# Optimization experiments

Measured on AMD Instinct MI355X. Metric: run time of the kernel, lower is better.

The kernel has to match this reference:

```python
import jax, jax.numpy as jnp
import numpy as np

B, S, D = 2, 2048, 4096
H, KV, HD = 32, 8, 128
THETA = 10000.0


def rotate_half(x):
    x1, x2 = x[..., : HD // 2], x[..., HD // 2 :]
    return jnp.concatenate((-x2, x1), axis=-1)


def setup_inputs() -> dict:
    key = jax.random.key(0)
    ks = jax.random.split(key, 8)
    s = 1.0 / np.sqrt(D)
    return {
        "hidden_states": jax.random.normal(ks[0], (B, S, D), jnp.float32),
        "modality_indicators": jax.random.randint(ks[1], (B, S), 0, 2, jnp.int64 if jax.config.jax_enable_x64 else jnp.int32),
        "position_ids": jnp.arange(S, dtype=jnp.int32),
        "Wq": jax.random.normal(ks[2], (D, H * HD), jnp.float32) * s,
        "Wk0": jax.random.normal(ks[3], (D, KV * HD), jnp.float32) * s,
        "Wk1": jax.random.normal(ks[4], (D, KV * HD), jnp.float32) * s,
        "Wv0": jax.random.normal(ks[5], (D, KV * HD), jnp.float32) * s,
        "Wv1": jax.random.normal(ks[6], (D, KV * HD), jnp.float32) * s,
        "Wo": jax.random.normal(ks[7], (H * HD, D), jnp.float32) * s,
    }


def reference(hidden_states, modality_indicators, position_ids, Wq, Wk0, Wk1, Wv0, Wv1, Wo):
    x = hidden_states
    # Multiway (modality-routed) k/v projections: per-token select between two linears.
    sel = (modality_indicators == 1)[..., None]  # [B,S,1]
    q = x @ Wq                                   # [B,S,H*HD]
    k = jnp.where(sel, x @ Wk1, x @ Wk0)         # [B,S,KV*HD]
    v = jnp.where(sel, x @ Wv1, x @ Wv0)

    q = q.reshape(B, S, H, HD).transpose(0, 2, 1, 3)    # [B,H,S,HD]
    k = k.reshape(B, S, KV, HD).transpose(0, 2, 1, 3)   # [B,KV,S,HD]
    v = v.reshape(B, S, KV, HD).transpose(0, 2, 1, 3)

    # RoPE cache and application (emb = cat(freqs, freqs))
    inv_freq = 1.0 / (THETA ** (jnp.arange(0, HD, 2, dtype=jnp.float32) / HD))
    freqs = position_ids.astype(jnp.float32)[:, None] * inv_freq[None, :]   # [S,HD/2]
    emb = jnp.concatenate((freqs, freqs), axis=-1)                          # [S,HD]
    cos = jnp.cos(emb)[None, None, :, :]                                    # [1,1,S,HD]
    sin = jnp.sin(emb)[None, None, :, :]
    q = q * cos + rotate_half(q) * sin
    k = k * cos + rotate_half(k) * sin

    # GQA: repeat kv heads
    n_rep = H // KV
    k = jnp.repeat(k, n_rep, axis=1)  # [B,H,S,HD]
    v = jnp.repeat(v, n_rep, axis=1)

    scores = jnp.einsum("bhqd,bhkd->bhqk", q, k) / np.sqrt(HD)
    causal = jnp.tril(jnp.ones((S, S), dtype=bool))
    scores = jnp.where(causal[None, None], scores, jnp.finfo(scores.dtype).min)
    attn = jax.nn.softmax(scores, axis=-1)
    ctx = jnp.einsum("bhqk,bhkd->bhqd", attn, v)            # [B,H,S,HD]
    ctx = ctx.transpose(0, 2, 1, 3).reshape(B, S, H * HD)
    return ctx @ Wo
```

## Files before the change

### kernel.cpp

```cpp
#include <hip/hip_runtime.h>

typedef unsigned short u16;
typedef unsigned int   u32;
using bf16x8 = __attribute__((ext_vector_type(8))) __bf16;
using f32x4  = __attribute__((ext_vector_type(4))) float;
using f32x16 = __attribute__((ext_vector_type(16))) float;
using u32x4  = __attribute__((ext_vector_type(4))) unsigned int;
using ushort8 = __attribute__((ext_vector_type(8))) unsigned short;


__device__ __forceinline__ u16 f2bf(float f) {
  u32 u = __builtin_bit_cast(u32, f);
  return (u16)((u + 0x7fffu + ((u >> 16) & 1u)) >> 16);
}
__device__ __forceinline__ float bf2f(u16 h) {
  return __builtin_bit_cast(float, (u32)h << 16);
}
__device__ __forceinline__ f32x4 mfma16(bf16x8 a, bf16x8 b, f32x4 c) {
  return __builtin_amdgcn_mfma_f32_16x16x32_bf16(a, b, c, 0, 0, 0);
}
__device__ __forceinline__ f32x16 mfma32(bf16x8 a, bf16x8 b, f32x16 c) {
  return __builtin_amdgcn_mfma_f32_32x32x16_bf16(a, b, c, 0, 0, 0);
}
__device__ __forceinline__ f32x16 zero16() {
  f32x16 z;
#pragma unroll
  for (int i = 0; i < 16; ++i) z[i] = 0.f;
  return z;
}
__device__ __forceinline__ void g2l16(const void* gp, void* lp) {
  __builtin_amdgcn_global_load_lds(
      (__attribute__((address_space(1))) void*)(void*)gp,
      (__attribute__((address_space(3))) void*)lp, 16, 0, 0);
}

__global__ void k_cvt(const float* __restrict__ in, u16* __restrict__ out, int n4) {
  int i = blockIdx.x * 256 + threadIdx.x;
  if (i >= n4) return;
  float4 v = ((const float4*)in)[i];
  ushort4 o;
  o.x = f2bf(v.x); o.y = f2bf(v.y); o.z = f2bf(v.z); o.w = f2bf(v.w);
  ((ushort4*)out)[i] = o;
}

__device__ __forceinline__ void tcvt_tile(const float* __restrict__ in, u16* __restrict__ out,
                                          int K, int N, int nt, int kt, u16 (*t)[72]) {
  const int n0 = nt * 64, k0 = kt * 64;
  const int tid = threadIdx.x;
  const int r = tid >> 2, c4 = (tid & 3) * 16;
  const float* src = in + (size_t)(k0 + r) * N + n0 + c4;
#pragma unroll
  for (int q = 0; q < 4; ++q) {
    float4 v = *(const float4*)(src + 4 * q);
    t[c4 + 4 * q + 0][r] = f2bf(v.x);
    t[c4 + 4 * q + 1][r] = f2bf(v.y);
    t[c4 + 4 * q + 2][r] = f2bf(v.z);
    t[c4 + 4 * q + 3][r] = f2bf(v.w);
  }
  __syncthreads();
  u16* dst = out + (size_t)(n0 + r) * K + k0 + c4;
#pragma unroll
  for (int hh = 0; hh < 2; ++hh)
    *(ushort8*)(dst + 8 * hh) = *(const ushort8*)(&t[r][c4 + 8 * hh]);
}

__global__ __launch_bounds__(256) void k_tcvt(const float* __restrict__ in, u16* __restrict__ out,
                                              int K, int N) {
  __shared__ u16 t[64][72];
  tcvt_tile(in, out, K, N, blockIdx.x, blockIdx.y, t);
}

__global__ __launch_bounds__(256) void k_tcvt5(const float* __restrict__ Wq, const float* __restrict__ Wk0,
                                               const float* __restrict__ Wv0, const float* __restrict__ Wk1,
                                               const float* __restrict__ Wv1, u16* __restrict__ WqT,
                                               u16* __restrict__ Wkv0T, u16* __restrict__ Wkv1T) {
  __shared__ u16 t[64][72];
  int bid = blockIdx.x;
  if (bid < 4096) {
    tcvt_tile(Wq, WqT, 4096, 4096, bid & 63, bid >> 6, t);
  } else {
    int r = bid - 4096;
    int mat = r >> 10, rr = r & 1023;
    const float* src = (mat == 0) ? Wk0 : (mat == 1) ? Wv0 : (mat == 2) ? Wk1 : Wv1;
    u16* dst = (mat == 0) ? Wkv0T : (mat == 1) ? (Wkv0T + (size_t)1024 * 4096)
                                  : (mat == 2) ? Wkv1T : (Wkv1T + (size_t)1024 * 4096);
    tcvt_tile(src, dst, 4096, 1024, rr & 15, rr >> 4, t);
  }
}

__global__ void k_scan(const int* __restrict__ mod, int* __restrict__ perm, int* __restrict__ meta) {
  __shared__ int ps[1024];
  const int b = blockIdx.x, t = threadIdx.x;
  perm[b * 2304 + t] = -1;
  perm[b * 2304 + 1024 + t] = -1;
  if (t < 256) perm[b * 2304 + 2048 + t] = -1;
  const int i0 = 2 * t, i1 = 2 * t + 1;
  const int f0 = (mod[b * 2048 + i0] != 1) ? 1 : 0;
  const int f1 = (mod[b * 2048 + i1] != 1) ? 1 : 0;
  const int sum = f0 + f1;
  ps[t] = sum;
  __syncthreads();
  for (int off = 1; off < 1024; off <<= 1) {
    int v = (t >= off) ? ps[t - off] : 0;
    __syncthreads();
    ps[t] += v;
    __syncthreads();
  }
  const int total0 = ps[1023];
  const int excl = ps[t] - sum;
  const int nt0 = (total0 + 255) >> 8;
  const int off1 = nt0 * 256;
  const int s0 = f0 ? excl : off1 + (i0 - excl);
  const int s1 = f1 ? (excl + f0) : off1 + (i1 - (excl + f0));
  perm[b * 2304 + s0] = i0;
  perm[b * 2304 + s1] = i1;
  if (t == 0) { meta[b * 2] = total0; meta[b * 2 + 1] = nt0; }
}

#define TILE_BODY(T, VMLIT, DOSTAGE)                                         \
  {                                                                          \
    asm volatile("s_waitcnt vmcnt(" VMLIT ")" ::: "memory");                 \
    __builtin_amdgcn_s_barrier();                                            \
    __builtin_amdgcn_sched_barrier(0);                                       \
    const u16* base_ = lds + ((T) & 3) * 16384;                              \
    bf16x8 bfr[4], afr[4];                                                   \
    _Pragma("unroll")                                                        \
    for (int nf = 0; nf < 4; ++nf)                                           \
      bfr[nf] = *(const bf16x8*)(base_ + boff + nf * 512);                   \
    _Pragma("unroll")                                                        \
    for (int mf = 0; mf < 4; ++mf)                                           \
      afr[mf] = *(const bf16x8*)(base_ + aoff + mf * 512);                   \
    if (DOSTAGE) stage((T) + 3);                                             \
    __builtin_amdgcn_s_setprio(1);                                           \
    _Pragma("unroll")                                                        \
    for (int mf = 0; mf < 4; ++mf)                                           \
      _Pragma("unroll")                                                      \
      for (int nf = 0; nf < 4; ++nf)                                         \
        acc[mf][nf] = mfma16(afr[mf], bfr[nf], acc[mf][nf]);                 \
    __builtin_amdgcn_s_setprio(0);                                           \
  }

#define GEMM_MAIN_LOOP()                                                     \
  stage(0); stage(1); stage(2);                                              \
  for (int t = 0; t < 125; ++t) TILE_BODY(t, "4", true);                     \
  TILE_BODY(125, "4", false);                                                \
  TILE_BODY(126, "2", false);                                                \
  TILE_BODY(127, "0", false);

__global__ __launch_bounds__(1024, 4) void k_gemm8(const u16* __restrict__ A, const u16* __restrict__ Bt,
                                                   float* __restrict__ Cp) {
  __shared__ u16 lds[4 * 16384];
  const int tid = threadIdx.x, wid = tid >> 6, l = tid & 63, g = l >> 4, li = l & 15;
  const int wr = wid >> 2, wc = wid & 3;
  const int bid = blockIdx.x;
  const int swz = (bid & 7) * 32 + (bid >> 3);
  const int m0 = (swz >> 4) * 256, n0 = (swz & 15) * 256;

  const int srow = wid * 16 + (l >> 2);
  const int sgg = (l & 3) ^ ((l >> 3) & 3);
  const u16* pA = A + (size_t)(m0 + srow) * 4096 + sgg * 8;
  const u16* pB = Bt + (size_t)(n0 + srow) * 4096 + sgg * 8;

  auto stage = [&](int t) {
    u16* da = (u16*)lds + (t & 3) * 16384 + wid * 512;
    g2l16(pA + t * 32, da);
    g2l16(pB + t * 32, da + 8192);
  };

  const int lsl8 = (g ^ ((li >> 1) & 3)) * 8;
  const int aoff = (wr * 64 + li) * 32 + lsl8;
  const int boff = 8192 + (wc * 64 + li) * 32 + lsl8;

  const f32x4 vzero = {0.f, 0.f, 0.f, 0.f};
  f32x4 acc[4][4];
#pragma unroll
  for (int m = 0; m < 4; ++m)
#pragma unroll
    for (int n = 0; n < 4; ++n) acc[m][n] = vzero;

  GEMM_MAIN_LOOP();

#pragma unroll
  for (int mf = 0; mf < 4; ++mf)
#pragma unroll
    for (int nf = 0; nf < 4; ++nf)
#pragma unroll
      for (int j = 0; j < 4; ++j) {
        int row = m0 + wr * 64 + mf * 16 + g * 4 + j;
        int col = n0 + wc * 64 + nf * 16 + li;
        Cp[(size_t)row * 4096 + col] = acc[mf][nf][j];
      }
}

__global__ __launch_bounds__(1024, 4) void k_gemmQKV(const u16* __restrict__ Xb, const u16* __restrict__ WqT,
                                                     const u16* __restrict__ B0, const u16* __restrict__ B1,
                                                     const int* __restrict__ perm, const int* __restrict__ meta,
                                                     u16* __restrict__ Qr, u16* __restrict__ Ksel,
                                                     u16* __restrict__ Vsel) {
  __shared__ u16 lds[4 * 16384];
  const int tid = threadIdx.x, wid = tid >> 6, l = tid & 63, g = l >> 4, li = l & 15;
  const int wr = wid >> 2, wc = wid & 3;
  const int bid = blockIdx.x;
  const bool isQ = bid < 256;

  const int srow = wid * 16 + (l >> 2);
  const int sgg = (l & 3) ^ ((l >> 3) & 3);

  int m0 = 0, n0 = 0, bb = 0, tm = 0;
  const u16 *pA, *pB;
  if (isQ) {
    const int swz = (bid & 7) * 32 + (bid >> 3);
    m0 = (swz >> 4) * 256; n0 = (swz & 15) * 256;
    pA = Xb + (size_t)(m0 + srow) * 4096 + sgg * 8;
    pB = WqT + (size_t)(n0 + srow) * 4096 + sgg * 8;
  } else {
    const int kb = bid - 256;
    const int seg = kb >> 3;
    n0 = (kb & 7) * 256;
    bb = seg / 9; tm = seg % 9;
    const int nt0 = meta[bb * 2 + 1];
    const u16* Bt = (tm >= nt0) ? B1 : B0;
    int t0 = perm[bb * 2304 + tm * 256 + srow];
    if (t0 < 0) t0 = 0;
    pA = Xb + ((size_t)bb * 2048 + t0) * 4096 + sgg * 8;
    pB = Bt + (size_t)(n0 + srow) * 4096 + sgg * 8;
  }

  auto stage = [&](int t) {
    u16* da = (u16*)lds + (t & 3) * 16384 + wid * 512;
    g2l16(pA + t * 32, da);
    g2l16(pB + t * 32, da + 8192);
  };

  const int lsl8 = (g ^ ((li >> 1) & 3)) * 8;
  const int aoff = (wr * 64 + li) * 32 + lsl8;
  const int boff = 8192 + (wc * 64 + li) * 32 + lsl8;

  const f32x4 vzero = {0.f, 0.f, 0.f, 0.f};
  f32x4 acc[4][4];
#pragma unroll
  for (int m = 0; m < 4; ++m)
#pragma unroll
    for (int n = 0; n < 4; ++n) acc[m][n] = vzero;

  GEMM_MAIN_LOOP();

  if (isQ) {
#pragma unroll
    for (int mf = 0; mf < 4; ++mf)
#pragma unroll
      for (int nf = 0; nf < 4; ++nf)
#pragma unroll
        for (int j = 0; j < 4; ++j) {
          int row = m0 + wr * 64 + mf * 16 + g * 4 + j;
          int col = n0 + wc * 64 + nf * 16 + li;
          int b = row >> 11, s = row & 2047, h = col >> 7, d = col & 127;
          Qr[(((size_t)(b * 32 + h)) * 2048 + s) * 128 + d] = f2bf(acc[mf][nf][j]);
        }
  } else {
#pragma unroll
    for (int mf = 0; mf < 4; ++mf)
#pragma unroll
      for (int nf = 0; nf < 4; ++nf)
#pragma unroll
        for (int j = 0; j < 4; ++j) {
          int slot = tm * 256 + wr * 64 + mf * 16 + g * 4 + j;
          int tok = perm[bb * 2304 + slot];
          if (tok >= 0) {
            int col = n0 + wc * 64 + nf * 16 + li;
            int kv = col >> 10, hh = (col >> 7) & 7, d = col & 127;
            u16* dst = (kv ? Vsel : Ksel) + (((size_t)(bb * 8 + hh)) * 2048 + tok) * 128 + d;
            *dst = f2bf(acc[mf][nf][j]);
          }
        }
  }
}

__global__ __launch_bounds__(256) void k_ropekv(u16* __restrict__ Q, const u16* __restrict__ Ks,
                                                const u16* __restrict__ Vs, const int* __restrict__ pos,
                                                u16* __restrict__ Kr, u16* __restrict__ Vt) {
  __shared__ u16 Vl[64][136];
  const int bid = blockIdx.x;
  const int tid = threadIdx.x, l = tid & 63;
  const float invf = expf((float)l * -0.14391156831212787f);
  if (bid < 32768) {
    int row = bid * 4 + (tid >> 6);
    int s = row & 2047;
    u16* p = Q + (size_t)row * 128;
    float x1 = bf2f(p[l]), x2 = bf2f(p[l + 64]);
    float ang = (float)pos[s] * invf;
    float cs = cosf(ang), sn = sinf(ang);
    const float sc = 0.08838834764831845f;
    p[l] = f2bf((x1 * cs - x2 * sn) * sc);
    p[l + 64] = f2bf((x2 * cs + x1 * sn) * sc);
  } else {
    int blk = bid - 32768;
    int st = blk & 31, kvh = (blk >> 5) & 7, b = blk >> 8;
    int s0 = st * 64;
    int wid = tid >> 6;
    size_t slab = (size_t)(b * 8 + kvh) * 2048;
    for (int rr = 0; rr < 16; ++rr) {
      int r = wid * 16 + rr;
      int s = s0 + r;
      const u16* ks = Ks + (slab + s) * 128;
      const u16* vs = Vs + (slab + s) * 128;
      float ang = (float)pos[s] * invf;
      float cs = cosf(ang), sn = sinf(ang);
      float x1 = bf2f(ks[l]), x2 = bf2f(ks[l + 64]);
      u16* kd = Kr + (slab + s) * 128;
      kd[l] = f2bf(x1 * cs - x2 * sn);
      kd[l + 64] = f2bf(x2 * cs + x1 * sn);
      Vl[r][l] = vs[l];
      Vl[r][l + 64] = vs[l + 64];
    }
    __syncthreads();
    int d = tid >> 1, si0 = (tid & 1) * 32;
    u16* vd = Vt + ((size_t)(b * 8 + kvh) * 128 + d) * 2048 + s0 + si0;
#pragma unroll
    for (int k4 = 0; k4 < 8; ++k4) {
      ushort4 o;
      o.x = Vl[si0 + k4 * 4 + 0][d];
      o.y = Vl[si0 + k4 * 4 + 1][d];
      o.z = Vl[si0 + k4 * 4 + 2][d];
      o.w = Vl[si0 + k4 * 4 + 3][d];
      *(ushort4*)(vd + k4 * 4) = o;
    }
  }
}

__global__ __launch_bounds__(256, 2) void k_attn(const u16* __restrict__ Q, const u16* __restrict__ Kr,
                                                 const u16* __restrict__ Vt, u16* __restrict__ ctx) {
  __shared__ u16 Kl[2 * 64 * 128];
  __shared__ u16 Vl[2 * 128 * 64];
  const int bh = blockIdx.x;
  const int p = blockIdx.y;
  const int b = bh >> 5, h = bh & 31, kvh = h >> 2;
  const int tid = threadIdx.x, w = tid >> 6, l = tid & 63;
  const int lo5 = l & 31, hi = l >> 5;
  const bool hib = hi != 0;
  const size_t kvslab = (size_t)(b * 8 + kvh) * 2048;
  const u16* Kg = Kr + kvslab * 128;
  const u16* Vg = Vt + kvslab * 128;
  const float L2E = 1.4426950408889634f;

  auto stage = [&](int kt, int bi) {
#pragma unroll
    for (int i = 0; i < 4; ++i) {
      int c = w * 4 + i;
      int slot = c * 1024 + l * 16;
      {
        int row = slot >> 8;
        int inner = (slot & 255) ^ ((row & 15) << 4);
        g2l16((const char*)Kg + kt * 16384 + row * 256 + inner,
              (char*)Kl + bi * 16384 + c * 1024);
      }
      {
        int row = slot >> 7;
        int inner = (slot & 127) ^ ((row & 7) << 4);
        g2l16((const char*)Vg + (size_t)row * 4096 + kt * 128 + inner,
              (char*)Vl + bi * 16384 + c * 1024);
      }
    }
  };

  for (int hf = 0; hf < 2; ++hf) {
    const int qi = hf ? (15 - p) : p;
    const int q0 = qi * 128;
    const int qlane = q0 + w * 32 + lo5;
    const u16* qrow = Q + ((size_t)bh * 2048 + qlane) * 128;
    bf16x8 qf[8];
#pragma unroll
    for (int kk = 0; kk < 8; ++kk) qf[kk] = *(const bf16x8*)(qrow + kk * 16 + hi * 8);

    f32x16 ot[4];
#pragma unroll
    for (int i = 0; i < 4; ++i) ot[i] = zero16();
    float m = -1e30f, ls = 0.f;

    const int nkt = 2 * qi + 2;
    stage(0, 0);
    stage(1, 1);
    for (int kt = 0; kt < nkt; ++kt) {
      if (kt + 1 < nkt) {
        asm volatile("s_waitcnt vmcnt(8)" ::: "memory");
      } else {
        asm volatile("s_waitcnt vmcnt(0)" ::: "memory");
      }
      __builtin_amdgcn_s_barrier();
      __builtin_amdgcn_sched_barrier(0);
      const char* kbase = (const char*)Kl + (kt & 1) * 16384;
      const char* vbase = (const char*)Vl + (kt & 1) * 16384;
      const int ktb = kt * 64;
      if (ktb <= q0 + w * 32 + 31) {
        f32x16 st[2];
        st[0] = zero16(); st[1] = zero16();
#pragma unroll
        for (int kk = 0; kk < 8; ++kk) {
          bf16x8 kfr[2];
#pragma unroll
          for (int mf = 0; mf < 2; ++mf) {
            int row = mf * 32 + lo5;
            kfr[mf] = *(const bf16x8*)(kbase + row * 256 + ((kk * 32 + hi * 16) ^ ((row & 15) << 4)));
          }
          __builtin_amdgcn_s_setprio(1);
          st[0] = mfma32(kfr[0], qf[kk], st[0]);
          st[1] = mfma32(kfr[1], qf[kk], st[1]);
          __builtin_amdgcn_s_setprio(0);
        }
        if (ktb + 63 > q0 + w * 32) {
#pragma unroll
          for (int mf = 0; mf < 2; ++mf)
#pragma unroll
            for (int r = 0; r < 16; ++r) {
              int kg = ktb + mf * 32 + (r & 3) + 8 * (r >> 2) + 4 * hi;
              if (kg > qlane) st[mf][r] = -3.0e38f;
            }
        }
        float t[16];
#pragma unroll
        for (int r = 0; r < 16; ++r) t[r] = fmaxf(st[0][r], st[1][r]);
#pragma unroll
        for (int s = 8; s >= 1; s >>= 1)
#pragma unroll
          for (int r = 0; r < s; ++r) t[r] = fmaxf(t[r], t[r + s]);
        float pmax = fmaxf(t[0], __shfl_xor(t[0], 32));
        if (!__all(pmax <= m + 8.f)) {
          float nm = fmaxf(m, pmax);
          float resc = exp2f((m - nm) * L2E);
          m = nm;
          ls *= resc;
#pragma unroll
          for (int i = 0; i < 4; ++i)
#pragma unroll
            for (int r = 0; r < 16; ++r) ot[i][r] *= resc;
        }
#pragma unroll
        for (int mf = 0; mf < 2; ++mf)
#pragma unroll
          for (int r = 0; r < 16; ++r) st[mf][r] = exp2f((st[mf][r] - m) * L2E);
        float u[16];
#pragma unroll
        for (int r = 0; r < 16; ++r) u[r] = st[0][r] + st[1][r];
#pragma unroll
        for (int s = 8; s >= 1; s >>= 1)
#pragma unroll
          for (int r = 0; r < s; ++r) u[r] += u[r + s];
        ls += u[0] + __shfl_xor(u[0], 32);
        u32 pkv[16];
#pragma unroll
        for (int mf = 0; mf < 2; ++mf)
#pragma unroll
          for (int tt = 0; tt < 8; ++tt) {
            u32 r;
            asm("v_cvt_pk_bf16_f32 %0, %1, %2" : "=v"(r) : "v"(st[mf][2 * tt]), "v"(st[mf][2 * tt + 1]));
            pkv[mf * 8 + tt] = r;
          }
        bf16x8 pfrag[4];
#pragma unroll
        for (int kk = 0; kk < 4; ++kk) {
          int c = (kk >> 1) * 8 + (kk & 1) * 4;
          u32 m0 = hib ? pkv[c + 2] : pkv[c + 0];
          u32 m1 = hib ? pkv[c + 3] : pkv[c + 1];
          u32 s0 = hib ? pkv[c + 0] : pkv[c + 2];
          u32 s1 = hib ? pkv[c + 1] : pkv[c + 3];
          u32 r0 = (u32)__shfl_xor((int)s0, 32);
          u32 r1 = (u32)__shfl_xor((int)s1, 32);
          u32x4 wv = {hib ? r0 : m0, hib ? r1 : m1, hib ? m0 : r0, hib ? m1 : r1};
          pfrag[kk] = __builtin_bit_cast(bf16x8, wv);
        }
#pragma unroll
        for (int mfV = 0; mfV < 4; ++mfV) {
          int row = mfV * 32 + lo5;
          const char* vb = vbase + row * 128;
          int sw = (row & 7) << 4;
          bf16x8 vf[4];
#pragma unroll
          for (int kk = 0; kk < 4; ++kk)
            vf[kk] = *(const bf16x8*)(vb + ((kk * 32 + hi * 16) ^ sw));
          __builtin_amdgcn_s_setprio(1);
#pragma unroll
          for (int kk = 0; kk < 4; ++kk) ot[mfV] = mfma32(vf[kk], pfrag[kk], ot[mfV]);
          __builtin_amdgcn_s_setprio(0);
        }
      }
      __builtin_amdgcn_s_barrier();
      if (kt + 2 < nkt) stage(kt + 2, kt & 1);
    }
    float inv = 1.0f / ls;
    u16* crow = ctx + ((size_t)(b * 2048) + qlane) * 4096 + h * 128;
#pragma unroll
    for (int mfV = 0; mfV < 4; ++mfV)
#pragma unroll
      for (int rq = 0; rq < 4; ++rq) {
        ushort4 o4;
        o4.x = f2bf(ot[mfV][rq * 4 + 0] * inv);
        o4.y = f2bf(ot[mfV][rq * 4 + 1] * inv);
        o4.z = f2bf(ot[mfV][rq * 4 + 2] * inv);
        o4.w = f2bf(ot[mfV][rq * 4 + 3] * inv);
        *(ushort4*)(crow + mfV * 32 + rq * 8 + hi * 4) = o4;
      }
  }
}

extern "C" void kernel_launch(void* const* d_in, const int* in_sizes, int n_in,
                              void* d_out, int out_size, void* d_ws, size_t ws_size,
                              hipStream_t stream) {
  (void)in_sizes; (void)n_in; (void)out_size; (void)ws_size;
  const float* X   = (const float*)d_in[0];
  const int*   mod = (const int*)d_in[1];
  const int*   pos = (const int*)d_in[2];
  const float* Wq  = (const float*)d_in[3];
  const float* Wk0 = (const float*)d_in[4];
  const float* Wk1 = (const float*)d_in[5];
  const float* Wv0 = (const float*)d_in[6];
  const float* Wv1 = (const float*)d_in[7];
  const float* Wo  = (const float*)d_in[8];
  float* out = (float*)d_out;

  u16* p = (u16*)d_ws;
  auto take = [&](size_t n) { u16* r = p; p += n; return r; };
  u16* Xb    = take(16777216);
  u16* WqT   = take(16777216);
  u16* WoT   = take(16777216);
  u16* Wkv0T = take(8388608);
  u16* Wkv1T = take(8388608);
  u16* Qr    = take(16777216);
  u16* Ksel  = take(4194304);
  u16* Vsel  = take(4194304);
  int* perm  = (int*)take(9216);
  int* meta  = (int*)take(64);
  u16* Kr  = WqT;
  u16* Vtr = WqT + 4194304;
  u16* ctx = Xb;

  k_cvt<<<dim3(16384), 256, 0, stream>>>(X, Xb, 4194304);
  k_scan<<<dim3(2), 1024, 0, stream>>>(mod, perm, meta);
  k_tcvt5<<<dim3(8192), 256, 0, stream>>>(Wq, Wk0, Wv0, Wk1, Wv1, WqT, Wkv0T, Wkv1T);

  k_gemmQKV<<<dim3(400), 1024, 0, stream>>>(Xb, WqT, Wkv0T, Wkv1T, perm, meta, Qr, Ksel, Vsel);

  k_ropekv<<<dim3(33280), 256, 0, stream>>>(Qr, Ksel, Vsel, pos, Kr, Vtr);

  k_attn<<<dim3(64, 8), 256, 0, stream>>>(Qr, Kr, Vtr, ctx);

  k_tcvt<<<dim3(64, 64), 256, 0, stream>>>(Wo, WoT, 4096, 4096);

  k_gemm8<<<dim3(256), 1024, 0, stream>>>(ctx, WoT, out);
}
```

Before: 550.7 us.

## Double-buffer QKV GEMM LDS and regroup attention blocks by KV head

The QKV projection GEMM moves from a 4-deep LDS ring with 3 tiles in flight to a 2-buffer scheme that stages the next-next tile after a second barrier, halving its shared memory footprint, which could raise occupancy but adds a barrier per tile and shortens prefetch distance. The attention launch becomes 1D with a block index mapping that places the four query heads sharing a KV head (and both batches) adjacently, aiming to improve L2 reuse of K/V tiles. Work per block is unchanged.

```diff
diff --git a/kernel.cpp b/kernel.cpp
--- a/kernel.cpp
+++ b/kernel.cpp
@@ -147,6 +147,36 @@
   TILE_BODY(126, "2", false);                                                \
   TILE_BODY(127, "0", false);
 
+#define TILE_BODY2(T, VMLIT, DOSTAGE)                                        \
+  {                                                                          \
+    asm volatile("s_waitcnt vmcnt(" VMLIT ")" ::: "memory");                 \
+    __builtin_amdgcn_s_barrier();                                            \
+    __builtin_amdgcn_sched_barrier(0);                                       \
+    const u16* base_ = lds + ((T) & 1) * 16384;                              \
+    bf16x8 bfr[4], afr[4];                                                   \
+    _Pragma("unroll")                                                        \
+    for (int nf = 0; nf < 4; ++nf)                                           \
+      bfr[nf] = *(const bf16x8*)(base_ + boff + nf * 512);                   \
+    _Pragma("unroll")                                                        \
+    for (int mf = 0; mf < 4; ++mf)                                           \
+      afr[mf] = *(const bf16x8*)(base_ + aoff + mf * 512);                   \
+    __builtin_amdgcn_s_setprio(1);                                           \
+    _Pragma("unroll")                                                        \
+    for (int mf = 0; mf < 4; ++mf)                                           \
+      _Pragma("unroll")                                                      \
+      for (int nf = 0; nf < 4; ++nf)                                         \
+        acc[mf][nf] = mfma16(afr[mf], bfr[nf], acc[mf][nf]);                 \
+    __builtin_amdgcn_s_setprio(0);                                           \
+    __builtin_amdgcn_s_barrier();                                            \
+    if (DOSTAGE) stage((T) + 2);                                             \
+  }
+
+#define GEMM_MAIN_LOOP2()                                                    \
+  stage(0); stage(1);                                                        \
+  for (int t = 0; t < 126; ++t) TILE_BODY2(t, "2", true);                    \
+  TILE_BODY2(126, "2", false);                                               \
+  TILE_BODY2(127, "0", false);
+
 __global__ __launch_bounds__(1024, 4) void k_gemm8(const u16* __restrict__ A, const u16* __restrict__ Bt,
                                                    float* __restrict__ Cp) {
   __shared__ u16 lds[4 * 16384];
@@ -197,7 +227,7 @@
                                                      const int* __restrict__ perm, const int* __restrict__ meta,
                                                      u16* __restrict__ Qr, u16* __restrict__ Ksel,
                                                      u16* __restrict__ Vsel) {
-  __shared__ u16 lds[4 * 16384];
+  __shared__ u16 lds[2 * 16384];
   const int tid = threadIdx.x, wid = tid >> 6, l = tid & 63, g = l >> 4, li = l & 15;
   const int wr = wid >> 2, wc = wid & 3;
   const int bid = blockIdx.x;
@@ -227,7 +257,7 @@
   }
 
   auto stage = [&](int t) {
-    u16* da = (u16*)lds + (t & 3) * 16384 + wid * 512;
+    u16* da = (u16*)lds + (t & 1) * 16384 + wid * 512;
     g2l16(pA + t * 32, da);
     g2l16(pB + t * 32, da + 8192);
   };
@@ -243,7 +273,7 @@
 #pragma unroll
     for (int n = 0; n < 4; ++n) acc[m][n] = vzero;
 
-  GEMM_MAIN_LOOP();
+  GEMM_MAIN_LOOP2();
 
   if (isQ) {
 #pragma unroll
@@ -332,9 +362,12 @@
                                                  const u16* __restrict__ Vt, u16* __restrict__ ctx) {
   __shared__ u16 Kl[2 * 64 * 128];
   __shared__ u16 Vl[2 * 128 * 64];
-  const int bh = blockIdx.x;
-  const int p = blockIdx.y;
-  const int b = bh >> 5, h = bh & 31, kvh = h >> 2;
+  const int id = blockIdx.x;
+  const int gkv = id & 15, j = id >> 4;
+  const int b = gkv >> 3, kvh = gkv & 7;
+  const int h = kvh * 4 + (j & 3);
+  const int p = j >> 2;
+  const int bh = b * 32 + h;
   const int tid = threadIdx.x, w = tid >> 6, l = tid & 63;
   const int lo5 = l & 31, hi = l >> 5;
   const bool hib = hi != 0;
@@ -541,7 +574,7 @@
 
   k_ropekv<<<dim3(33280), 256, 0, stream>>>(Qr, Ksel, Vsel, pos, Kr, Vtr);
 
-  k_attn<<<dim3(64, 8), 256, 0, stream>>>(Qr, Kr, Vtr, ctx);
+  k_attn<<<dim3(512), 256, 0, stream>>>(Qr, Kr, Vtr, ctx);
 
   k_tcvt<<<dim3(64, 64), 256, 0, stream>>>(Wo, WoT, 4096, 4096);
 
```

Result: slower. 566.1 us (+2.8%).

## Restructure GEMMs to 8-wave 256x256 tiles with quadrant-interleaved ping-pong pipeline

Applied to the files above, without the earlier changes.

Both GEMM kernels move from 16 waves with a four-deep single-stage pipeline to 8 waves that each compute a 128x64 sub-tile. The K step grows to 64 and LDS is split into two ping-pong buffers, with loads and MFMAs interleaved in quadrant order under barriers. The aim is more MFMA work per LDS read and finer-grained overlap of global-to-LDS copies with compute, at the cost of more accumulator registers per wave. Separately, the attention grid is flattened so the four query heads sharing a KV head launch next to each other, which should improve L2 reuse of K/V.

```diff
diff --git a/kernel.cpp b/kernel.cpp
--- a/kernel.cpp
+++ b/kernel.cpp
@@ -117,102 +117,142 @@
   if (t == 0) { meta[b * 2] = total0; meta[b * 2 + 1] = nt0; }
 }
 
-#define TILE_BODY(T, VMLIT, DOSTAGE)                                         \
-  {                                                                          \
-    asm volatile("s_waitcnt vmcnt(" VMLIT ")" ::: "memory");                 \
-    __builtin_amdgcn_s_barrier();                                            \
-    __builtin_amdgcn_sched_barrier(0);                                       \
-    const u16* base_ = lds + ((T) & 3) * 16384;                              \
-    bf16x8 bfr[4], afr[4];                                                   \
-    _Pragma("unroll")                                                        \
-    for (int nf = 0; nf < 4; ++nf)                                           \
-      bfr[nf] = *(const bf16x8*)(base_ + boff + nf * 512);                   \
-    _Pragma("unroll")                                                        \
-    for (int mf = 0; mf < 4; ++mf)                                           \
-      afr[mf] = *(const bf16x8*)(base_ + aoff + mf * 512);                   \
-    if (DOSTAGE) stage((T) + 3);                                             \
-    __builtin_amdgcn_s_setprio(1);                                           \
-    _Pragma("unroll")                                                        \
-    for (int mf = 0; mf < 4; ++mf)                                           \
-      _Pragma("unroll")                                                      \
-      for (int nf = 0; nf < 4; ++nf)                                         \
-        acc[mf][nf] = mfma16(afr[mf], bfr[nf], acc[mf][nf]);                 \
-    __builtin_amdgcn_s_setprio(0);                                           \
-  }
-
-#define GEMM_MAIN_LOOP()                                                     \
-  stage(0); stage(1); stage(2);                                              \
-  for (int t = 0; t < 125; ++t) TILE_BODY(t, "4", true);                     \
-  TILE_BODY(125, "4", false);                                                \
-  TILE_BODY(126, "2", false);                                                \
-  TILE_BODY(127, "0", false);
-
-__global__ __launch_bounds__(1024, 4) void k_gemm8(const u16* __restrict__ A, const u16* __restrict__ Bt,
-                                                   float* __restrict__ Cp) {
-  __shared__ u16 lds[4 * 16384];
+#define BARSB() { __builtin_amdgcn_s_barrier(); __builtin_amdgcn_sched_barrier(0); }
+#define VMC(N)  asm volatile("s_waitcnt vmcnt(" #N ")" ::: "memory")
+
+#define READ_A(MH, SL) { _Pragma("unroll") for (int mf_ = 0; mf_ < 4; ++mf_) {       \
+    const char* a_ = (const char*)lds8 + (SL)*65536 + (MH)*16384 + (arow + mf_*16)*128; \
+    afr[mf_][0] = *(const bf16x8*)(a_ + swc0);                                        \
+    afr[mf_][1] = *(const bf16x8*)(a_ + swc1); } }
+
+#define READ_B(NH, SL) { _Pragma("unroll") for (int nf_ = 0; nf_ < 2; ++nf_) {       \
+    const char* b_ = (const char*)lds8 + (SL)*65536 + 32768 + (NH)*16384 + (brow + nf_*16)*128; \
+    bfr[nf_][0] = *(const bf16x8*)(b_ + swc0);                                        \
+    bfr[nf_][1] = *(const bf16x8*)(b_ + swc1); } }
+
+#define MM16(MH, NH) { __builtin_amdgcn_s_setprio(1);                                 \
+  _Pragma("unroll") for (int mf_ = 0; mf_ < 4; ++mf_)                                 \
+    _Pragma("unroll") for (int nf_ = 0; nf_ < 2; ++nf_) {                             \
+      acc[MH][mf_][NH][nf_] = mfma16(afr[mf_][0], bfr[nf_][0], acc[MH][mf_][NH][nf_]); \
+      acc[MH][mf_][NH][nf_] = mfma16(afr[mf_][1], bfr[nf_][1], acc[MH][mf_][NH][nf_]); } \
+  __builtin_amdgcn_s_setprio(0); }
+
+#define STAGE_A(T, MH) { int ts_ = (T) < 64 ? (T) : 63;                               \
+    char* d_ = (char*)lds8 + ((T)&1)*65536 + (MH)*16384 + wid*1024;                   \
+    g2l16(pA0[MH] + ts_*64, d_); g2l16(pA1[MH] + ts_*64, d_ + 8192); }
+
+#define STAGE_B(T, NH) { int ts_ = (T) < 64 ? (T) : 63;                               \
+    char* d_ = (char*)lds8 + ((T)&1)*65536 + 32768 + (NH)*16384 + wid*1024;           \
+    g2l16(pB0[NH] + ts_*64, d_); g2l16(pB1[NH] + ts_*64, d_ + 8192); }
+
+#define G8_MAINLOOP()                                                                 \
+  STAGE_A(0,0); STAGE_B(0,1); STAGE_A(0,1); STAGE_B(0,0);                             \
+  STAGE_A(1,0); STAGE_B(1,1); STAGE_A(1,1);                                           \
+  VMC(6); BARSB();                                                                    \
+  for (int i_ = 0; i_ < 32; ++i_) {                                                   \
+    const int ta_ = 2 * i_;                                                           \
+    READ_A(0,0); READ_B(0,0); STAGE_B(ta_+1, 0); BARSB(); MM16(0,0); BARSB();         \
+    READ_B(1,0);              STAGE_A(ta_+2, 0); BARSB(); MM16(0,1); BARSB();         \
+    READ_A(1,0);              STAGE_B(ta_+2, 1); BARSB(); MM16(1,1); BARSB();         \
+    READ_B(0,0);              STAGE_A(ta_+2, 1); BARSB(); MM16(1,0); VMC(4); BARSB(); \
+    READ_A(0,1); READ_B(0,1); STAGE_B(ta_+2, 0); BARSB(); MM16(0,0); BARSB();         \
+    READ_B(1,1);              STAGE_A(ta_+3, 0); BARSB(); MM16(0,1); BARSB();         \
+    READ_A(1,1);              STAGE_B(ta_+3, 1); BARSB(); MM16(1,1); BARSB();         \
+    READ_B(0,1);              STAGE_A(ta_+3, 1); BARSB(); MM16(1,0); VMC(4); BARSB(); \
+  }
+
+__global__ __launch_bounds__(512, 2) void k_gemm8(const u16* __restrict__ A, const u16* __restrict__ Bt,
+                                                  float* __restrict__ Cp) {
+  __shared__ u16 lds8[65536];
   const int tid = threadIdx.x, wid = tid >> 6, l = tid & 63, g = l >> 4, li = l & 15;
   const int wr = wid >> 2, wc = wid & 3;
   const int bid = blockIdx.x;
   const int swz = (bid & 7) * 32 + (bid >> 3);
   const int m0 = (swz >> 4) * 256, n0 = (swz & 15) * 256;
 
-  const int srow = wid * 16 + (l >> 2);
-  const int sgg = (l & 3) ^ ((l >> 3) & 3);
-  const u16* pA = A + (size_t)(m0 + srow) * 4096 + sgg * 8;
-  const u16* pB = Bt + (size_t)(n0 + srow) * 4096 + sgg * 8;
-
-  auto stage = [&](int t) {
-    u16* da = (u16*)lds + (t & 3) * 16384 + wid * 512;
-    g2l16(pA + t * 32, da);
-    g2l16(pB + t * 32, da + 8192);
-  };
-
-  const int lsl8 = (g ^ ((li >> 1) & 3)) * 8;
-  const int aoff = (wr * 64 + li) * 32 + lsl8;
-  const int boff = 8192 + (wc * 64 + li) * 32 + lsl8;
-
+  const int swc0 = (g * 16) ^ ((li & 7) << 4);
+  const int swc1 = (64 + g * 16) ^ ((li & 7) << 4);
+  const int arow = wr * 64 + li;
+  const int brow = wc * 32 + li;
+
+  const int l8a = tid * 16, l8b = 8192 + tid * 16;
+  const int oa = l8a ^ (((l8a >> 7) & 7) << 4), ob = l8b ^ (((l8b >> 7) & 7) << 4);
+  const int rl0 = oa >> 7, cb0 = oa & 127, rl1 = ob >> 7, cb1 = ob & 127;
+  const int RA0 = (rl0 >> 6) * 128 + (rl0 & 63), RA1 = (rl1 >> 6) * 128 + (rl1 & 63);
+  const int CB0 = (rl0 >> 5) * 64 + (rl0 & 31), CB1 = (rl1 >> 5) * 64 + (rl1 & 31);
+  const u16 *pA0[2], *pA1[2], *pB0[2], *pB1[2];
+#pragma unroll
+  for (int mh = 0; mh < 2; ++mh) {
+    pA0[mh] = A + (size_t)(m0 + RA0 + mh * 64) * 4096 + cb0 / 2;
+    pA1[mh] = A + (size_t)(m0 + RA1 + mh * 64) * 4096 + cb1 / 2;
+    pB0[mh] = Bt + (size_t)(n0 + CB0 + mh * 32) * 4096 + cb0 / 2;
+    pB1[mh] = Bt + (size_t)(n0 + CB1 + mh * 32) * 4096 + cb1 / 2;
+  }
+
+  bf16x8 afr[4][2], bfr[2][2];
   const f32x4 vzero = {0.f, 0.f, 0.f, 0.f};
-  f32x4 acc[4][4];
-#pragma unroll
-  for (int m = 0; m < 4; ++m)
-#pragma unroll
-    for (int n = 0; n < 4; ++n) acc[m][n] = vzero;
-
-  GEMM_MAIN_LOOP();
-
-#pragma unroll
-  for (int mf = 0; mf < 4; ++mf)
-#pragma unroll
-    for (int nf = 0; nf < 4; ++nf)
-#pragma unroll
-      for (int j = 0; j < 4; ++j) {
-        int row = m0 + wr * 64 + mf * 16 + g * 4 + j;
-        int col = n0 + wc * 64 + nf * 16 + li;
-        Cp[(size_t)row * 4096 + col] = acc[mf][nf][j];
-      }
-}
-
-__global__ __launch_bounds__(1024, 4) void k_gemmQKV(const u16* __restrict__ Xb, const u16* __restrict__ WqT,
-                                                     const u16* __restrict__ B0, const u16* __restrict__ B1,
-                                                     const int* __restrict__ perm, const int* __restrict__ meta,
-                                                     u16* __restrict__ Qr, u16* __restrict__ Ksel,
-                                                     u16* __restrict__ Vsel) {
-  __shared__ u16 lds[4 * 16384];
+  f32x4 acc[2][4][2][2];
+#pragma unroll
+  for (int a = 0; a < 2; ++a)
+#pragma unroll
+    for (int b = 0; b < 4; ++b)
+#pragma unroll
+      for (int c = 0; c < 2; ++c)
+#pragma unroll
+        for (int d = 0; d < 2; ++d) acc[a][b][c][d] = vzero;
+
+  G8_MAINLOOP();
+
+#pragma unroll
+  for (int mh = 0; mh < 2; ++mh)
+#pragma unroll
+    for (int mf = 0; mf < 4; ++mf)
+#pragma unroll
+      for (int nh = 0; nh < 2; ++nh)
+#pragma unroll
+        for (int nf = 0; nf < 2; ++nf)
+#pragma unroll
+          for (int j = 0; j < 4; ++j) {
+            int row = m0 + wr * 128 + mh * 64 + mf * 16 + g * 4 + j;
+            int col = n0 + wc * 64 + nh * 32 + nf * 16 + li;
+            Cp[(size_t)row * 4096 + col] = acc[mh][mf][nh][nf][j];
+          }
+}
+
+__global__ __launch_bounds__(512, 2) void k_gemmQKV(const u16* __restrict__ Xb, const u16* __restrict__ WqT,
+                                                    const u16* __restrict__ B0, const u16* __restrict__ B1,
+                                                    const int* __restrict__ perm, const int* __restrict__ meta,
+                                                    u16* __restrict__ Qr, u16* __restrict__ Ksel,
+                                                    u16* __restrict__ Vsel) {
+  __shared__ u16 lds8[65536];
   const int tid = threadIdx.x, wid = tid >> 6, l = tid & 63, g = l >> 4, li = l & 15;
   const int wr = wid >> 2, wc = wid & 3;
   const int bid = blockIdx.x;
   const bool isQ = bid < 256;
 
-  const int srow = wid * 16 + (l >> 2);
-  const int sgg = (l & 3) ^ ((l >> 3) & 3);
+  const int swc0 = (g * 16) ^ ((li & 7) << 4);
+  const int swc1 = (64 + g * 16) ^ ((li & 7) << 4);
+  const int arow = wr * 64 + li;
+  const int brow = wc * 32 + li;
+
+  const int l8a = tid * 16, l8b = 8192 + tid * 16;
+  const int oa = l8a ^ (((l8a >> 7) & 7) << 4), ob = l8b ^ (((l8b >> 7) & 7) << 4);
+  const int rl0 = oa >> 7, cb0 = oa & 127, rl1 = ob >> 7, cb1 = ob & 127;
+  const int RA0 = (rl0 >> 6) * 128 + (rl0 & 63), RA1 = (rl1 >> 6) * 128 + (rl1 & 63);
+  const int CB0 = (rl0 >> 5) * 64 + (rl0 & 31), CB1 = (rl1 >> 5) * 64 + (rl1 & 31);
 
   int m0 = 0, n0 = 0, bb = 0, tm = 0;
-  const u16 *pA, *pB;
+  const u16 *pA0[2], *pA1[2], *pB0[2], *pB1[2];
   if (isQ) {
     const int swz = (bid & 7) * 32 + (bid >> 3);
     m0 = (swz >> 4) * 256; n0 = (swz & 15) * 256;
-    pA = Xb + (size_t)(m0 + srow) * 4096 + sgg * 8;
-    pB = WqT + (size_t)(n0 + srow) * 4096 + sgg * 8;
+#pragma unroll
+    for (int mh = 0; mh < 2; ++mh) {
+      pA0[mh] = Xb + (size_t)(m0 + RA0 + mh * 64) * 4096 + cb0 / 2;
+      pA1[mh] = Xb + (size_t)(m0 + RA1 + mh * 64) * 4096 + cb1 / 2;
+      pB0[mh] = WqT + (size_t)(n0 + CB0 + mh * 32) * 4096 + cb0 / 2;
+      pB1[mh] = WqT + (size_t)(n0 + CB1 + mh * 32) * 4096 + cb1 / 2;
+    }
   } else {
     const int kb = bid - 256;
     const int seg = kb >> 3;
@@ -220,59 +260,68 @@
     bb = seg / 9; tm = seg % 9;
     const int nt0 = meta[bb * 2 + 1];
     const u16* Bt = (tm >= nt0) ? B1 : B0;
-    int t0 = perm[bb * 2304 + tm * 256 + srow];
-    if (t0 < 0) t0 = 0;
-    pA = Xb + ((size_t)bb * 2048 + t0) * 4096 + sgg * 8;
-    pB = Bt + (size_t)(n0 + srow) * 4096 + sgg * 8;
-  }
-
-  auto stage = [&](int t) {
-    u16* da = (u16*)lds + (t & 3) * 16384 + wid * 512;
-    g2l16(pA + t * 32, da);
-    g2l16(pB + t * 32, da + 8192);
-  };
-
-  const int lsl8 = (g ^ ((li >> 1) & 3)) * 8;
-  const int aoff = (wr * 64 + li) * 32 + lsl8;
-  const int boff = 8192 + (wc * 64 + li) * 32 + lsl8;
-
+    const int pbase = bb * 2304 + tm * 256;
+#pragma unroll
+    for (int mh = 0; mh < 2; ++mh) {
+      int t0 = perm[pbase + RA0 + mh * 64]; if (t0 < 0) t0 = 0;
+      int t1 = perm[pbase + RA1 + mh * 64]; if (t1 < 0) t1 = 0;
+      pA0[mh] = Xb + ((size_t)bb * 2048 + t0) * 4096 + cb0 / 2;
+      pA1[mh] = Xb + ((size_t)bb * 2048 + t1) * 4096 + cb1 / 2;
+      pB0[mh] = Bt + (size_t)(n0 + CB0 + mh * 32) * 4096 + cb0 / 2;
+      pB1[mh] = Bt + (size_t)(n0 + CB1 + mh * 32) * 4096 + cb1 / 2;
+    }
+  }
+
+  bf16x8 afr[4][2], bfr[2][2];
   const f32x4 vzero = {0.f, 0.f, 0.f, 0.f};
-  f32x4 acc[4][4];
-#pragma unroll
-  for (int m = 0; m < 4; ++m)
-#pragma unroll
-    for (int n = 0; n < 4; ++n) acc[m][n] = vzero;
-
-  GEMM_MAIN_LOOP();
+  f32x4 acc[2][4][2][2];
+#pragma unroll
+  for (int a = 0; a < 2; ++a)
+#pragma unroll
+    for (int b = 0; b < 4; ++b)
+#pragma unroll
+      for (int c = 0; c < 2; ++c)
+#pragma unroll
+        for (int d = 0; d < 2; ++d) acc[a][b][c][d] = vzero;
+
+  G8_MAINLOOP();
 
   if (isQ) {
 #pragma unroll
-    for (int mf = 0; mf < 4; ++mf)
-#pragma unroll
-      for (int nf = 0; nf < 4; ++nf)
-#pragma unroll
-        for (int j = 0; j < 4; ++j) {
-          int row = m0 + wr * 64 + mf * 16 + g * 4 + j;
-          int col = n0 + wc * 64 + nf * 16 + li;
-          int b = row >> 11, s = row & 2047, h = col >> 7, d = col & 127;
-          Qr[(((size_t)(b * 32 + h)) * 2048 + s) * 128 + d] = f2bf(acc[mf][nf][j]);
-        }
+    for (int mh = 0; mh < 2; ++mh)
+#pragma unroll
+      for (int mf = 0; mf < 4; ++mf)
+#pragma unroll
+        for (int nh = 0; nh < 2; ++nh)
+#pragma unroll
+          for (int nf = 0; nf < 2; ++nf)
+#pragma unroll
+            for (int j = 0; j < 4; ++j) {
+              int row = m0 + wr * 128 + mh * 64 + mf * 16 + g * 4 + j;
+              int col = n0 + wc * 64 + nh * 32 + nf * 16 + li;
+              int b = row >> 11, s = row & 2047, h = col >> 7, d = col & 127;
+              Qr[(((size_t)(b * 32 + h)) * 2048 + s) * 128 + d] = f2bf(acc[mh][mf][nh][nf][j]);
+            }
   } else {
 #pragma unroll
-    for (int mf = 0; mf < 4; ++mf)
-#pragma unroll
-      for (int nf = 0; nf < 4; ++nf)
-#pragma unroll
-        for (int j = 0; j < 4; ++j) {
-          int slot = tm * 256 + wr * 64 + mf * 16 + g * 4 + j;
-          int tok = perm[bb * 2304 + slot];
-          if (tok >= 0) {
-            int col = n0 + wc * 64 + nf * 16 + li;
-            int kv = col >> 10, hh = (col >> 7) & 7, d = col & 127;
-            u16* dst = (kv ? Vsel : Ksel) + (((size_t)(bb * 8 + hh)) * 2048 + tok) * 128 + d;
-            *dst = f2bf(acc[mf][nf][j]);
-          }
-        }
+    for (int mh = 0; mh < 2; ++mh)
+#pragma unroll
+      for (int mf = 0; mf < 4; ++mf)
+#pragma unroll
+        for (int nh = 0; nh < 2; ++nh)
+#pragma unroll
+          for (int nf = 0; nf < 2; ++nf)
+#pragma unroll
+            for (int j = 0; j < 4; ++j) {
+              int slot = tm * 256 + wr * 128 + mh * 64 + mf * 16 + g * 4 + j;
+              int tok = perm[bb * 2304 + slot];
+              if (tok >= 0) {
+                int col = n0 + wc * 64 + nh * 32 + nf * 16 + li;
+                int kv = col >> 10, hh = (col >> 7) & 7, d = col & 127;
+                u16* dst = (kv ? Vsel : Ksel) + (((size_t)(bb * 8 + hh)) * 2048 + tok) * 128 + d;
+                *dst = f2bf(acc[mh][mf][nh][nf][j]);
+              }
+            }
   }
 }
 
@@ -332,9 +381,12 @@
                                                  const u16* __restrict__ Vt, u16* __restrict__ ctx) {
   __shared__ u16 Kl[2 * 64 * 128];
   __shared__ u16 Vl[2 * 128 * 64];
-  const int bh = blockIdx.x;
-  const int p = blockIdx.y;
-  const int b = bh >> 5, h = bh & 31, kvh = h >> 2;
+  const int id = blockIdx.x;
+  const int gkv = id & 15, j = id >> 4;
+  const int b = gkv >> 3, kvh = gkv & 7;
+  const int h = kvh * 4 + (j & 3);
+  const int p = j >> 2;
+  const int bh = b * 32 + h;
   const int tid = threadIdx.x, w = tid >> 6, l = tid & 63;
   const int lo5 = l & 31, hi = l >> 5;
   const bool hib = hi != 0;
@@ -537,13 +589,13 @@
   k_scan<<<dim3(2), 1024, 0, stream>>>(mod, perm, meta);
   k_tcvt5<<<dim3(8192), 256, 0, stream>>>(Wq, Wk0, Wv0, Wk1, Wv1, WqT, Wkv0T, Wkv1T);
 
-  k_gemmQKV<<<dim3(400), 1024, 0, stream>>>(Xb, WqT, Wkv0T, Wkv1T, perm, meta, Qr, Ksel, Vsel);
+  k_gemmQKV<<<dim3(400), 512, 0, stream>>>(Xb, WqT, Wkv0T, Wkv1T, perm, meta, Qr, Ksel, Vsel);
 
   k_ropekv<<<dim3(33280), 256, 0, stream>>>(Qr, Ksel, Vsel, pos, Kr, Vtr);
 
-  k_attn<<<dim3(64, 8), 256, 0, stream>>>(Qr, Kr, Vtr, ctx);
+  k_attn<<<dim3(512), 256, 0, stream>>>(Qr, Kr, Vtr, ctx);
 
   k_tcvt<<<dim3(64, 64), 256, 0, stream>>>(Wo, WoT, 4096, 4096);
 
-  k_gemm8<<<dim3(256), 1024, 0, stream>>>(ctx, WoT, out);
-}
+  k_gemm8<<<dim3(256), 512, 0, stream>>>(ctx, WoT, out);
+}
```

Result: faster. 530.5 us (-3.7%).
